# Kernel tuning notes

Measured on AMD Instinct MI355X. Metric: run time of the kernel, lower is better.

The kernel has to match this reference:

```python
import jax, jax.numpy as jnp
import numpy as np

DIM = 8          # per-head dim
ATT_EPS = 1e-15
BN_EPS = 1e-6


def setup_inputs() -> dict:
    key = jax.random.key(0)
    ks = jax.random.split(key, 6)
    B, C, H, W = 8, 256, 64, 64
    td = 256                      # heads * dim = 32 * 8
    return {
        'x':      jax.random.normal(ks[0], (B, C, H, W), jnp.float32),
        'w_qkv':  jax.random.normal(ks[1], (3 * td, C), jnp.float32) * 0.05,
        'w_dw':   jax.random.normal(ks[2], (3 * td, 1, 5, 5), jnp.float32) * 0.05,
        'w_pw':   jax.random.normal(ks[3], (96, 8, 8), jnp.float32) * 0.05,   # (groups, out/g, in/g)
        'w_proj': jax.random.normal(ks[4], (C, 2 * td), jnp.float32) * 0.05,
        'bn_gamma': jnp.ones((C,), jnp.float32),
        'bn_beta':  jnp.zeros((C,), jnp.float32),
        'bn_mean':  jnp.zeros((C,), jnp.float32),
        'bn_var':   jnp.ones((C,), jnp.float32),
    }


def _relu_linear_att(ms, H, W):
    # ms: [B, C, H, W] with C = heads * 3*DIM
    B = ms.shape[0]
    d = DIM
    qkv = ms.reshape(B, -1, 3 * d, H * W).transpose(0, 1, 3, 2)   # [B, h, N, 3d]
    q = jax.nn.relu(qkv[..., :d])
    k = jax.nn.relu(qkv[..., d:2 * d])
    v = qkv[..., 2 * d:]
    v = jnp.pad(v, ((0, 0), (0, 0), (0, 0), (0, 1)), constant_values=1.0)  # ones column
    kv = jnp.einsum('bhnd,bhne->bhde', k, v)                       # [B, h, d, d+1]
    out = jnp.einsum('bhnd,bhde->bhne', q, kv)                     # [B, h, N, d+1]
    out = out[..., :-1] / (out[..., -1:] + ATT_EPS)
    return out.transpose(0, 1, 3, 2).reshape(B, -1, H, W)          # [B, h*d, H, W]


def reference(x, w_qkv, w_dw, w_pw, w_proj, bn_gamma, bn_beta, bn_mean, bn_var):
    B, C, H, W = x.shape
    # 1x1 qkv projection
    qkv = jnp.einsum('oc,bchw->bohw', w_qkv, x)                    # [B, 768, H, W]
    # multiscale aggregation: 5x5 depthwise then grouped 1x1 (groups = 3*heads = 96)
    dw = jax.lax.conv_general_dilated(
        qkv, w_dw, window_strides=(1, 1), padding=[(2, 2), (2, 2)],
        dimension_numbers=('NCHW', 'OIHW', 'NCHW'),
        feature_group_count=qkv.shape[1])
    G, O, I = w_pw.shape
    agg = jnp.einsum('goi,bgihw->bgohw', w_pw,
                     dw.reshape(B, G, I, H, W)).reshape(B, G * O, H, W)
    ms = jnp.concatenate([qkv, agg], axis=1)                       # [B, 1536, H, W]
    att = _relu_linear_att(ms, H, W)                               # [B, 512, H, W]
    # proj: 1x1 conv + BatchNorm (eval mode) + identity activation
    p = jnp.einsum('oc,bchw->bohw', w_proj, att)                   # [B, 256, H, W]
    inv = bn_gamma / jnp.sqrt(bn_var + BN_EPS)
    p = p * inv[None, :, None, None] + (bn_beta - bn_mean * inv)[None, :, None, None]
    return x + p
```

## Files before the change

kernel.cpp:

```cpp
#include <hip/hip_runtime.h>
#include <hip/hip_bf16.h>


#define HW 4096
#define ATT_EPS 1e-15f
#define BN_EPS 1e-6f

typedef __attribute__((ext_vector_type(8))) short short8;
typedef __attribute__((ext_vector_type(4))) short short4v;
typedef __attribute__((ext_vector_type(4))) float f32x4;
typedef __attribute__((ext_vector_type(8))) unsigned short u16x8;
typedef __attribute__((ext_vector_type(4))) unsigned short u16x4;

static __device__ inline short f2bf(float f) {
    union { float f; unsigned u; } v; v.f = f;
    unsigned r = v.u + 0x7fff + ((v.u >> 16) & 1);
    return (short)(r >> 16);
}
static __device__ inline float bf2f(unsigned short u) {
    union { unsigned u; float f; } v; v.u = (unsigned)u << 16; return v.f;
}

__global__ __launch_bounds__(256) void prep_w(const float* __restrict__ wproj,
                                              unsigned short* __restrict__ wbf) {
    const int i = (blockIdx.x * 256 + threadIdx.x) * 4;
    float4 v = *(const float4*)&wproj[i];
    u16x4 r = {(unsigned short)f2bf(v.x), (unsigned short)f2bf(v.y),
               (unsigned short)f2bf(v.z), (unsigned short)f2bf(v.w)};
    *(u16x4*)&wbf[i] = r;
}

__global__ __launch_bounds__(256) void qkv_gemm(const float* __restrict__ x,
                                                const float* __restrict__ w,
                                                unsigned short* __restrict__ qkv) {
    __shared__ short A_l[128 * 40];
    __shared__ short B_l[128 * 40];
    const int t  = threadIdx.x;
    const int b  = blockIdx.z;
    const int ob = blockIdx.y * 128;
    const int nb = blockIdx.x * 128;
    const float* xb = x + (size_t)b * 256 * HW;

    const int lane = t & 63, wave = t >> 6;
    const int wo = (wave >> 1) * 64, wn = (wave & 1) * 64;

    f32x4 acc[4][4];
#pragma unroll
    for (int s = 0; s < 4; s++)
#pragma unroll
        for (int u = 0; u < 4; u++) acc[s][u] = (f32x4){0.f, 0.f, 0.f, 0.f};

    const int col4 = (t & 7) * 4;
    const int r0   = t >> 3;
    for (int kb = 0; kb < 256; kb += 32) {
        __syncthreads();
#pragma unroll
        for (int i = 0; i < 4; i++) {
            const int r = r0 + 32 * i;
            float4 v = *(const float4*)&w[(ob + r) * 256 + kb + col4];
            short4v s4 = {f2bf(v.x), f2bf(v.y), f2bf(v.z), f2bf(v.w)};
            *(short4v*)&A_l[r * 40 + col4] = s4;
        }
#pragma unroll
        for (int i = 0; i < 4; i++) {
            const int n4 = (t & 7) + 8 * i;
            float4 v = *(const float4*)&xb[(size_t)(kb + r0) * HW + nb + n4 * 4];
            B_l[(n4 * 4 + 0) * 40 + r0] = f2bf(v.x);
            B_l[(n4 * 4 + 1) * 40 + r0] = f2bf(v.y);
            B_l[(n4 * 4 + 2) * 40 + r0] = f2bf(v.z);
            B_l[(n4 * 4 + 3) * 40 + r0] = f2bf(v.w);
        }
        __syncthreads();

        short8 af[4], bf[4];
#pragma unroll
        for (int s = 0; s < 4; s++)
            af[s] = *(const short8*)&A_l[(wo + s * 16 + (lane & 15)) * 40 + (lane >> 4) * 8];
#pragma unroll
        for (int u = 0; u < 4; u++)
            bf[u] = *(const short8*)&B_l[(wn + u * 16 + (lane & 15)) * 40 + (lane >> 4) * 8];
#pragma unroll
        for (int s = 0; s < 4; s++)
#pragma unroll
            for (int u = 0; u < 4; u++)
                acc[s][u] = __builtin_amdgcn_mfma_f32_16x16x32_bf16(af[s], bf[u], acc[s][u], 0, 0, 0);
    }

#pragma unroll
    for (int s = 0; s < 4; s++)
#pragma unroll
        for (int u = 0; u < 4; u++)
#pragma unroll
            for (int r = 0; r < 4; r++) {
                const int o = ob + wo + s * 16 + (lane >> 4) * 4 + r;
                const int n = nb + wn + u * 16 + (lane & 15);
                qkv[((size_t)b * 768 + o) * HW + n] = (unsigned short)f2bf(acc[s][u][r]);
            }
}

__global__ __launch_bounds__(256, 3) void dw_agg(const unsigned short* __restrict__ qkv,
                                                 const float* __restrict__ wdw,
                                                 const float* __restrict__ wpw,
                                                 unsigned short* __restrict__ agg) {
    __shared__ float tile_raw[4 + 8 * 20 * 64 + 4];
    __shared__ float wk[8][25];
    __shared__ float pw[64];
    float* base = tile_raw + 4;
    const int b = blockIdx.z, g = blockIdx.y;
    const int y0 = blockIdx.x * 16;
    const int t = threadIdx.x;

    if (t < 200) wk[t / 25][t % 25] = wdw[(g * 8) * 25 + t];
    if (t < 64)  pw[t] = wpw[g * 64 + t];

#pragma unroll
    for (int k = 0; k < 5; k++) {
        const int i = t + 256 * k;
        const int c8 = i & 7, rr = (i >> 3) % 20, ch = i / 160;
        const int y = y0 - 2 + rr;
        u16x8 v = {0, 0, 0, 0, 0, 0, 0, 0};
        if (y >= 0 && y < 64)
            v = *(const u16x8*)&qkv[((size_t)(b * 768 + g * 8 + ch)) * HW + y * 64 + c8 * 8];
        f32x4 lo = {bf2f(v[0]), bf2f(v[1]), bf2f(v[2]), bf2f(v[3])};
        f32x4 hi = {bf2f(v[4]), bf2f(v[5]), bf2f(v[6]), bf2f(v[7])};
        *(f32x4*)&base[i * 8]     = lo;
        *(f32x4*)&base[i * 8 + 4] = hi;
    }
    __syncthreads();

    const int tx = t & 15, ty = t >> 4;
    float out[8][4];
#pragma unroll
    for (int o = 0; o < 8; o++)
#pragma unroll
        for (int j = 0; j < 4; j++) out[o][j] = 0.f;

#pragma unroll 1
    for (int ch = 0; ch < 8; ch++) {
        float a0 = 0.f, a1 = 0.f, a2 = 0.f, a3 = 0.f;
#pragma unroll
        for (int dy = 0; dy < 5; dy++) {
            const int off = ch * 1280 + (ty + dy) * 64 + tx * 4;
            f32x4 L  = *(const f32x4*)&base[off - 4];
            f32x4 C  = *(const f32x4*)&base[off];
            f32x4 R  = *(const f32x4*)&base[off + 4];
            float win[8];
            win[0] = (tx == 0)  ? 0.f : L[2];
            win[1] = (tx == 0)  ? 0.f : L[3];
            win[2] = C[0]; win[3] = C[1];
            win[4] = C[2]; win[5] = C[3];
            win[6] = (tx == 15) ? 0.f : R[0];
            win[7] = (tx == 15) ? 0.f : R[1];
#pragma unroll
            for (int dx = 0; dx < 5; dx++) {
                const float wv = wk[ch][dy * 5 + dx];
                a0 += wv * win[dx + 0];
                a1 += wv * win[dx + 1];
                a2 += wv * win[dx + 2];
                a3 += wv * win[dx + 3];
            }
        }
#pragma unroll
        for (int o = 0; o < 8; o++) {
            const float wv = pw[o * 8 + ch];
            out[o][0] += wv * a0; out[o][1] += wv * a1;
            out[o][2] += wv * a2; out[o][3] += wv * a3;
        }
    }

#pragma unroll
    for (int o = 0; o < 8; o++) {
        u16x4 rv = {(unsigned short)f2bf(out[o][0]), (unsigned short)f2bf(out[o][1]),
                    (unsigned short)f2bf(out[o][2]), (unsigned short)f2bf(out[o][3])};
        *(u16x4*)&agg[((size_t)(b * 768 + g * 8 + o)) * HW + (y0 + ty) * 64 + tx * 4] = rv;
    }
}

__global__ __launch_bounds__(256) void kv_pass(const unsigned short* __restrict__ qkv,
                                               const unsigned short* __restrict__ agg,
                                               float* __restrict__ kvout) {
    const int h = blockIdx.x, b = blockIdx.y;
    const unsigned short* buf = (h < 32) ? qkv : agg;
    const int cbase = (h < 32) ? h * 24 : (h - 32) * 24;
    const u16x4* kp4 = (const u16x4*)(buf + ((size_t)b * 768 + cbase + 8)  * HW);
    const u16x4* vp4 = (const u16x4*)(buf + ((size_t)b * 768 + cbase + 16) * HW);

    float acc[8][9];
#pragma unroll
    for (int d = 0; d < 8; d++)
#pragma unroll
        for (int e = 0; e < 9; e++) acc[d][e] = 0.f;

#pragma unroll
    for (int k = 0; k < 4; k++) {
        const int nn = threadIdx.x + k * 256;
        float kk[8][4];
#pragma unroll
        for (int d = 0; d < 8; d++) {
            u16x4 v = kp4[d * 1024 + nn];
            kk[d][0] = fmaxf(bf2f(v.x), 0.f); kk[d][1] = fmaxf(bf2f(v.y), 0.f);
            kk[d][2] = fmaxf(bf2f(v.z), 0.f); kk[d][3] = fmaxf(bf2f(v.w), 0.f);
        }
#pragma unroll
        for (int e = 0; e < 8; e++) {
            u16x4 vr = vp4[e * 1024 + nn];
            float v0 = bf2f(vr.x), v1 = bf2f(vr.y), v2 = bf2f(vr.z), v3 = bf2f(vr.w);
#pragma unroll
            for (int d = 0; d < 8; d++)
                acc[d][e] += kk[d][0] * v0 + kk[d][1] * v1 + kk[d][2] * v2 + kk[d][3] * v3;
        }
#pragma unroll
        for (int d = 0; d < 8; d++)
            acc[d][8] += kk[d][0] + kk[d][1] + kk[d][2] + kk[d][3];
    }

    __shared__ float red[4][72];
    const int lane = threadIdx.x & 63, wv = threadIdx.x >> 6;
#pragma unroll
    for (int d = 0; d < 8; d++) {
#pragma unroll
        for (int e = 0; e < 9; e++) {
            float v = acc[d][e];
            v += __shfl_xor(v, 1);  v += __shfl_xor(v, 2);
            v += __shfl_xor(v, 4);  v += __shfl_xor(v, 8);
            v += __shfl_xor(v, 16); v += __shfl_xor(v, 32);
            if (lane == 0) red[wv][d * 9 + e] = v;
        }
    }
    __syncthreads();
    if (threadIdx.x < 72) {
        float s = red[0][threadIdx.x] + red[1][threadIdx.x] +
                  red[2][threadIdx.x] + red[3][threadIdx.x];
        kvout[((size_t)(b * 64 + h)) * 72 + threadIdx.x] = s;
    }
}

__global__ __launch_bounds__(256) void att_pass(const unsigned short* __restrict__ qkv,
                                                const unsigned short* __restrict__ agg,
                                                const float* __restrict__ kvbuf,
                                                unsigned short* __restrict__ att_f) {
    __shared__ float kvl[72];
    const int h = blockIdx.y, b = blockIdx.z;
    const int t = threadIdx.x;
    if (t < 72) kvl[t] = kvbuf[((size_t)(b * 64 + h)) * 72 + t];
    __syncthreads();

    const unsigned short* buf = (h < 32) ? qkv : agg;
    const int cbase = (h & 31) * 24;
    const int n0 = (blockIdx.x * 256 + t) * 8;
    const unsigned short* qp = buf + ((size_t)b * 768 + cbase) * HW + n0;

    float q[8][8];
#pragma unroll
    for (int d = 0; d < 8; d++) {
        u16x8 v = *(const u16x8*)&qp[(size_t)d * HW];
#pragma unroll
        for (int j = 0; j < 8; j++) q[d][j] = fmaxf(bf2f(v[j]), 0.f);
    }

    unsigned short* op = att_f + (((size_t)(b * 64 + h)) * HW + n0) * 8;
#pragma unroll
    for (int j = 0; j < 8; j++) {
        float num[9];
#pragma unroll
        for (int e = 0; e < 9; e++) num[e] = 0.f;
#pragma unroll
        for (int d = 0; d < 8; d++) {
            const float qv = q[d][j];
            const float* kvh = &kvl[d * 9];
#pragma unroll
            for (int e = 0; e < 9; e++) num[e] += qv * kvh[e];
        }
        const float rden = 1.f / (num[8] + ATT_EPS);
        u16x8 r;
#pragma unroll
        for (int e = 0; e < 8; e++) r[e] = (unsigned short)f2bf(num[e] * rden);
        *(u16x8*)&op[j * 8] = r;
    }
}

__global__ __launch_bounds__(256) void proj_gemm(const unsigned short* __restrict__ wbf,
                                                 const unsigned short* __restrict__ att_f,
                                                 const float* __restrict__ gamma,
                                                 const float* __restrict__ beta,
                                                 const float* __restrict__ mean,
                                                 const float* __restrict__ var,
                                                 const float* __restrict__ x,
                                                 float* __restrict__ out) {
    const int t  = threadIdx.x;
    const int b  = blockIdx.z;
    const int ob = blockIdx.y * 128;
    const int nb = blockIdx.x * 128;
    const int lane = t & 63, wave = t >> 6;
    const int wo = (wave >> 1) * 64, wn = (wave & 1) * 64;

    const int am = lane & 15, ak = lane >> 4;
    const unsigned short* ap0 = wbf + (size_t)(ob + wo + am) * 512 + ak * 8;
    const unsigned short* bp0 = att_f +
        (((size_t)b * 64 + ak) * HW + nb + wn + am) * 8;

    f32x4 acc[4][4];
#pragma unroll
    for (int s = 0; s < 4; s++)
#pragma unroll
        for (int u = 0; u < 4; u++) acc[s][u] = (f32x4){0.f, 0.f, 0.f, 0.f};

    for (int kb = 0; kb < 512; kb += 32) {
        short8 af[4], bf[4];
#pragma unroll
        for (int s = 0; s < 4; s++)
            af[s] = *(const short8*)(ap0 + (size_t)s * 16 * 512 + kb);
#pragma unroll
        for (int u = 0; u < 4; u++)
            bf[u] = *(const short8*)(bp0 + ((size_t)(kb >> 3) * HW + u * 16) * 8);
#pragma unroll
        for (int s = 0; s < 4; s++)
#pragma unroll
            for (int u = 0; u < 4; u++)
                acc[s][u] = __builtin_amdgcn_mfma_f32_16x16x32_bf16(af[s], bf[u], acc[s][u], 0, 0, 0);
    }

#pragma unroll
    for (int s = 0; s < 4; s++) {
        const int o_base = ob + wo + s * 16 + (lane >> 4) * 4;
#pragma unroll
        for (int r = 0; r < 4; r++) {
            const int o = o_base + r;
            const float inv = gamma[o] * rsqrtf(var[o] + BN_EPS);
            const float sh  = beta[o] - mean[o] * inv;
#pragma unroll
            for (int u = 0; u < 4; u++) {
                const int n = nb + wn + u * 16 + (lane & 15);
                const size_t idx = ((size_t)b * 256 + o) * HW + n;
                out[idx] = x[idx] + acc[s][u][r] * inv + sh;
            }
        }
    }
}

extern "C" void kernel_launch(void* const* d_in, const int* in_sizes, int n_in,
                              void* d_out, int out_size, void* d_ws, size_t ws_size,
                              hipStream_t stream) {
    const float* x      = (const float*)d_in[0];
    const float* w_qkv  = (const float*)d_in[1];
    const float* w_dw   = (const float*)d_in[2];
    const float* w_pw   = (const float*)d_in[3];
    const float* w_proj = (const float*)d_in[4];
    const float* gamma  = (const float*)d_in[5];
    const float* beta   = (const float*)d_in[6];
    const float* mean   = (const float*)d_in[7];
    const float* var    = (const float*)d_in[8];
    float* out = (float*)d_out;

    unsigned short* qkv  = (unsigned short*)d_ws;
    unsigned short* agg  = qkv + (size_t)25165824;
    unsigned short* attf = agg + (size_t)25165824;
    unsigned short* wbf  = attf + (size_t)16777216;
    float* kvb = (float*)(wbf + (size_t)131072);

    prep_w  <<<dim3(128),       256, 0, stream>>>(w_proj, wbf);
    qkv_gemm<<<dim3(32, 6, 8),  256, 0, stream>>>(x, w_qkv, qkv);
    dw_agg  <<<dim3(4, 96, 8),  256, 0, stream>>>(qkv, w_dw, w_pw, agg);
    kv_pass <<<dim3(64, 8),     256, 0, stream>>>(qkv, agg, kvb);
    att_pass<<<dim3(2, 64, 8),  256, 0, stream>>>(qkv, agg, kvb, attf);
    proj_gemm<<<dim3(32, 2, 8), 256, 0, stream>>>(wbf, attf,
                                                  gamma, beta, mean, var, x, out);
}
```

Measured before the change: 249.6 us.

## Halve dw_agg LDS tile by staging channels in two halves; use shuffles for halo

The depthwise+grouped-pointwise kernel now loads its 8-channel input tile in two passes of 4 channels, cutting shared memory per block roughly in half. The launch bound rises from 3 to 6 blocks per SM to raise occupancy. Horizontal neighbor values come from lane shuffles within 16-lane rows instead of two extra LDS vector reads. The cost is an extra barrier and a serialized second load phase, and the higher occupancy target may squeeze registers and cause spills.

```diff
diff --git a/kernel.cpp b/kernel.cpp
--- a/kernel.cpp
+++ b/kernel.cpp
@@ -98,14 +98,13 @@
             }
 }
 
-__global__ __launch_bounds__(256, 3) void dw_agg(const unsigned short* __restrict__ qkv,
+__global__ __launch_bounds__(256, 6) void dw_agg(const unsigned short* __restrict__ qkv,
                                                  const float* __restrict__ wdw,
                                                  const float* __restrict__ wpw,
                                                  unsigned short* __restrict__ agg) {
-    __shared__ float tile_raw[4 + 8 * 20 * 64 + 4];
+    __shared__ float tile[4 * 20 * 64];
     __shared__ float wk[8][25];
     __shared__ float pw[64];
-    float* base = tile_raw + 4;
     const int b = blockIdx.z, g = blockIdx.y;
     const int y0 = blockIdx.x * 16;
     const int t = threadIdx.x;
@@ -113,21 +112,6 @@
     if (t < 200) wk[t / 25][t % 25] = wdw[(g * 8) * 25 + t];
     if (t < 64)  pw[t] = wpw[g * 64 + t];
 
-#pragma unroll
-    for (int k = 0; k < 5; k++) {
-        const int i = t + 256 * k;
-        const int c8 = i & 7, rr = (i >> 3) % 20, ch = i / 160;
-        const int y = y0 - 2 + rr;
-        u16x8 v = {0, 0, 0, 0, 0, 0, 0, 0};
-        if (y >= 0 && y < 64)
-            v = *(const u16x8*)&qkv[((size_t)(b * 768 + g * 8 + ch)) * HW + y * 64 + c8 * 8];
-        f32x4 lo = {bf2f(v[0]), bf2f(v[1]), bf2f(v[2]), bf2f(v[3])};
-        f32x4 hi = {bf2f(v[4]), bf2f(v[5]), bf2f(v[6]), bf2f(v[7])};
-        *(f32x4*)&base[i * 8]     = lo;
-        *(f32x4*)&base[i * 8 + 4] = hi;
-    }
-    __syncthreads();
-
     const int tx = t & 15, ty = t >> 4;
     float out[8][4];
 #pragma unroll
@@ -136,35 +120,59 @@
         for (int j = 0; j < 4; j++) out[o][j] = 0.f;
 
 #pragma unroll 1
-    for (int ch = 0; ch < 8; ch++) {
-        float a0 = 0.f, a1 = 0.f, a2 = 0.f, a3 = 0.f;
-#pragma unroll
-        for (int dy = 0; dy < 5; dy++) {
-            const int off = ch * 1280 + (ty + dy) * 64 + tx * 4;
-            f32x4 L  = *(const f32x4*)&base[off - 4];
-            f32x4 C  = *(const f32x4*)&base[off];
-            f32x4 R  = *(const f32x4*)&base[off + 4];
-            float win[8];
-            win[0] = (tx == 0)  ? 0.f : L[2];
-            win[1] = (tx == 0)  ? 0.f : L[3];
-            win[2] = C[0]; win[3] = C[1];
-            win[4] = C[2]; win[5] = C[3];
-            win[6] = (tx == 15) ? 0.f : R[0];
-            win[7] = (tx == 15) ? 0.f : R[1];
-#pragma unroll
-            for (int dx = 0; dx < 5; dx++) {
-                const float wv = wk[ch][dy * 5 + dx];
-                a0 += wv * win[dx + 0];
-                a1 += wv * win[dx + 1];
-                a2 += wv * win[dx + 2];
-                a3 += wv * win[dx + 3];
-            }
-        }
-#pragma unroll
-        for (int o = 0; o < 8; o++) {
-            const float wv = pw[o * 8 + ch];
-            out[o][0] += wv * a0; out[o][1] += wv * a1;
-            out[o][2] += wv * a2; out[o][3] += wv * a3;
+    for (int half = 0; half < 2; half++) {
+        if (half) __syncthreads();
+#pragma unroll
+        for (int k = 0; k < 3; k++) {
+            const int i = t + 256 * k;
+            if (i < 640) {
+                const int c8 = i & 7, rr = (i >> 3) % 20, ch = i / 160;
+                const int y = y0 - 2 + rr;
+                u16x8 v = {0, 0, 0, 0, 0, 0, 0, 0};
+                if (y >= 0 && y < 64)
+                    v = *(const u16x8*)&qkv[((size_t)(b * 768 + g * 8 + half * 4 + ch)) * HW + y * 64 + c8 * 8];
+                f32x4 lo = {bf2f(v[0]), bf2f(v[1]), bf2f(v[2]), bf2f(v[3])};
+                f32x4 hi = {bf2f(v[4]), bf2f(v[5]), bf2f(v[6]), bf2f(v[7])};
+                *(f32x4*)&tile[i * 8]     = lo;
+                *(f32x4*)&tile[i * 8 + 4] = hi;
+            }
+        }
+        __syncthreads();
+
+#pragma unroll 1
+        for (int ch4 = 0; ch4 < 4; ch4++) {
+            const int ch = half * 4 + ch4;
+            float a0 = 0.f, a1 = 0.f, a2 = 0.f, a3 = 0.f;
+#pragma unroll
+            for (int dy = 0; dy < 5; dy++) {
+                const int off = ch4 * 1280 + (ty + dy) * 64 + tx * 4;
+                f32x4 C = *(const f32x4*)&tile[off];
+                const float l2 = __shfl_up(C[2], 1, 16);
+                const float l3 = __shfl_up(C[3], 1, 16);
+                const float r0v = __shfl_down(C[0], 1, 16);
+                const float r1v = __shfl_down(C[1], 1, 16);
+                float win[8];
+                win[0] = (tx == 0)  ? 0.f : l2;
+                win[1] = (tx == 0)  ? 0.f : l3;
+                win[2] = C[0]; win[3] = C[1];
+                win[4] = C[2]; win[5] = C[3];
+                win[6] = (tx == 15) ? 0.f : r0v;
+                win[7] = (tx == 15) ? 0.f : r1v;
+#pragma unroll
+                for (int dx = 0; dx < 5; dx++) {
+                    const float wv = wk[ch][dy * 5 + dx];
+                    a0 += wv * win[dx + 0];
+                    a1 += wv * win[dx + 1];
+                    a2 += wv * win[dx + 2];
+                    a3 += wv * win[dx + 3];
+                }
+            }
+#pragma unroll
+            for (int o = 0; o < 8; o++) {
+                const float wv = pw[o * 8 + ch];
+                out[o][0] += wv * a0; out[o][1] += wv * a1;
+                out[o][2] += wv * a2; out[o][3] += wv * a3;
+            }
         }
     }
 
```

Result: slower. 255.1 us (+2.2%).
